# Kernel optimization log

Measured on AMD Instinct MI355X. Metric: run time of the kernel, lower is better.

The kernel has to match this reference:

```python
import jax, jax.numpy as jnp
import numpy as np

T, B, K = 512, 512, 8
V, H, NL, NLAB = 5, 30, 4, 3


def setup_inputs() -> dict:
    key = jax.random.key(0)
    ks = jax.random.split(key, 12)
    s = 0.1
    return {
        "x": jax.random.randint(ks[0], (T, B, K), 0, V),
        "weight_of_x": jax.random.uniform(ks[1], (T, B, K), dtype=jnp.float32),
        "embed": jax.random.normal(ks[2], (V, H), dtype=jnp.float32) * s,
        "lstm_Wih": jax.random.normal(ks[3], (NL, 4 * H, H), dtype=jnp.float32) * s,
        "lstm_Whh": jax.random.normal(ks[4], (NL, 4 * H, H), dtype=jnp.float32) * s,
        "lstm_bih": jax.random.normal(ks[5], (NL, 4 * H), dtype=jnp.float32) * s,
        "lstm_bhh": jax.random.normal(ks[6], (NL, 4 * H), dtype=jnp.float32) * s,
        "attn_W1": jax.random.normal(ks[7], (H, 64), dtype=jnp.float32) * s,
        "attn_b1": jnp.zeros((64,), jnp.float32),
        "attn_W2": jax.random.normal(ks[8], (64, 1), dtype=jnp.float32) * s,
        "attn_b2": jnp.zeros((1,), jnp.float32),
        "fc_W": jax.random.normal(ks[9], (H, NLAB), dtype=jnp.float32) * s,
        "fc_b": jnp.zeros((NLAB,), jnp.float32),
    }


def _lstm_layer(xs, Wih, Whh, bih, bhh):
    # xs: (T, B, H_in); PyTorch gate order i, f, g, o
    b = bih + bhh
    Bsz = xs.shape[1]
    h0 = jnp.zeros((Bsz, Whh.shape[1]), xs.dtype)

    def step(carry, xt):
        h, c = carry
        gates = xt @ Wih.T + h @ Whh.T + b  # (B, 4H)
        i, f, g, o = jnp.split(gates, 4, axis=-1)
        i, f, o = jax.nn.sigmoid(i), jax.nn.sigmoid(f), jax.nn.sigmoid(o)
        g = jnp.tanh(g)
        c = f * c + i * g
        h = o * jnp.tanh(c)
        return (h, c), h

    _, hs = jax.lax.scan(step, (h0, h0), xs)
    return hs  # (T, B, H)


def reference(x, weight_of_x, embed, lstm_Wih, lstm_Whh, lstm_bih, lstm_bhh,
              attn_W1, attn_b1, attn_W2, attn_b2, fc_W, fc_b):
    # embedding + weighted mean pooling over K
    e = embed[x] * weight_of_x[..., None]          # (T, B, K, H)
    e = jax.nn.relu(e)
    seq = jnp.mean(e, axis=2)                      # (T, B, H)

    # 4-layer LSTM (loop over fixed num_layers)
    out = seq
    for l in range(lstm_Wih.shape[0]):
        out = _lstm_layer(out, lstm_Wih[l], lstm_Whh[l], lstm_bih[l], lstm_bhh[l])

    # attention pooling over time
    enc = jnp.transpose(out, (1, 0, 2))            # (B, T, H)
    energy = jax.nn.relu(enc @ attn_W1 + attn_b1) @ attn_W2 + attn_b2  # (B, T, 1)
    weights = jax.nn.softmax(energy[..., 0], axis=1)  # (B, T)
    pooled = jnp.sum(enc * weights[..., None], axis=1)  # (B, H)

    # dropout is identity in eval mode
    logit = jax.nn.softmax(pooled @ fc_W + fc_b, axis=1)  # (B, 3)
    return logit
```

## Files before the change

### kernel.cpp

```cpp
#include <hip/hip_runtime.h>

#define TT 512
#define BB 512
#define KK 8
#define HH 30
#define GG 120
#define NLAYER 4

typedef _Float16 half2v __attribute__((ext_vector_type(2)));

__device__ __forceinline__ float rcp_f(float x) { return __builtin_amdgcn_rcpf(x); }
__device__ __forceinline__ float rdlane_f(float v, int l) {
    return __int_as_float(__builtin_amdgcn_readlane(__float_as_int(v), l));
}
__device__ __forceinline__ unsigned int rdlane_u(unsigned int v, int l) {
    return (unsigned int)__builtin_amdgcn_readlane((int)v, l);
}
__device__ __forceinline__ half2v as_h2(unsigned int u) {
    union { unsigned int u; half2v h; } c; c.u = u; return c.h;
}
__device__ __forceinline__ float2 pk_fma_s(float2 a, float2 bs, float2 c) {
    float2 d;
    asm("v_pk_fma_f32 %0, %1, %2, %3" : "=v"(d) : "v"(a), "s"(bs), "v"(c));
    return d;
}
__device__ __forceinline__ float swap32_hi(float x) {
    float a = x, b = x;
    asm("v_permlane32_swap_b32 %0, %1" : "+v"(a), "+v"(b));
    return b;
}

__global__ __launch_bounds__(256) __attribute__((amdgpu_waves_per_eu(2, 2)))
void rnn_fused(
    const int*   __restrict__ xin,  const float* __restrict__ wxin,
    const float* __restrict__ embed,
    const float* __restrict__ Wih,  const float* __restrict__ Whh,
    const float* __restrict__ bih,  const float* __restrict__ bhh,
    const float* __restrict__ W1,   const float* __restrict__ b1,
    const float* __restrict__ W2,   const float* __restrict__ b2,
    const float* __restrict__ fcW,  const float* __restrict__ fcb,
    float* __restrict__ out)
{
    __shared__ alignas(16) float hstore[TT * HH];
    __shared__ alignas(16) unsigned int seqring16[2][16][16];
    __shared__ alignas(16) int   ringx[4][16][KK];
    __shared__ alignas(16) float ringw[4][16][KK];
    __shared__ alignas(16) unsigned int hring16[3][16][16];
    __shared__ alignas(16) float re_s[5 * HH];
    __shared__ alignas(16) float energy_s[TT];
    __shared__ float red_s[16];
    __shared__ float part_s[8][HH];
    __shared__ float pooled_s[HH];
    __shared__ float logits_s[3];
    __shared__ int   sync_s[8];

    const int tid  = threadIdx.x;
    const int wv   = tid >> 6;
    const int lane = tid & 63;
    const int b    = blockIdx.x;
    volatile int* vs = sync_s;

    if (tid < 8) sync_s[tid] = 0;
    if (tid < 5 * HH) re_s[tid] = fmaxf(embed[tid], 0.0f);

    int4 hx = {0,0,0,0}; float4 hw = {0,0,0,0};
    if (wv == 0 && lane < 32) {
        const int r = lane >> 1, hf = lane & 1;
        #pragma unroll
        for (int cc = 0; cc < 2; ++cc) {
            long off = ((long)(16 * cc + r) * BB + b) * KK + hf * 4;
            *(int4*)(&ringx[cc][r][hf * 4])   = *(const int4*)(xin  + off);
            *(float4*)(&ringw[cc][r][hf * 4]) = *(const float4*)(wxin + off);
        }
        long off2 = ((long)(32 + r) * BB + b) * KK + hf * 4;
        hx = *(const int4*)(xin  + off2);
        hw = *(const float4*)(wxin + off2);
    }

    const int half = lane >> 5;
    const int q31  = lane & 31;
    const int qq   = (q31 < HH) ? q31 : (HH - 1);
    const int rA   = qq + half * HH;
    const int rB   = rA + 60;
    half2v wihA_h[15], wihB_h[15], whhA_h[15], whhB_h[15];
    {
        const float* WihL = Wih + wv * GG * HH;
        const float* WhhL = Whh + wv * GG * HH;
        #pragma unroll
        for (int kk = 0; kk < 15; ++kk) {
            float2 a0 = *(const float2*)(WihL + rA * HH + 2 * kk);
            float2 a1 = *(const float2*)(WihL + rB * HH + 2 * kk);
            float2 a2 = *(const float2*)(WhhL + rA * HH + 2 * kk);
            float2 a3 = *(const float2*)(WhhL + rB * HH + 2 * kk);
            wihA_h[kk][0] = (_Float16)a0.x; wihA_h[kk][1] = (_Float16)a0.y;
            wihB_h[kk][0] = (_Float16)a1.x; wihB_h[kk][1] = (_Float16)a1.y;
            whhA_h[kk][0] = (_Float16)a2.x; whhA_h[kk][1] = (_Float16)a2.y;
            whhB_h[kk][0] = (_Float16)a3.x; whhB_h[kk][1] = (_Float16)a3.y;
        }
    }
    const float biasA = bih[wv * GG + rA] + bhh[wv * GG + rA];
    const float biasB = bih[wv * GG + rB] + bhh[wv * GG + rB];
    const float mBneg = (lane < 32) ? -2.0f : -1.0f;
    const float aB    = (lane < 32) ?  2.0f :  1.0f;
    const float dB    = (lane < 32) ? -1.0f :  0.0f;

    __syncthreads();

    float c_val = 0.0f;
    unsigned int hpk = 0;

    auto do_step = [&](int t) {
        const unsigned int* xsrc = (wv == 0) ? &seqring16[(t >> 4) & 1][t & 15][0]
                                             : &hring16[wv - 1][t & 15][0];
        uint4 q0 = ((const uint4*)xsrc)[0];
        uint4 q1 = ((const uint4*)xsrc)[1];
        uint4 q2 = ((const uint4*)xsrc)[2];
        uint4 q3 = ((const uint4*)xsrc)[3];
        const unsigned int xu[16] = {q0.x,q0.y,q0.z,q0.w, q1.x,q1.y,q1.z,q1.w,
                                     q2.x,q2.y,q2.z,q2.w, q3.x,q3.y,q3.z,q3.w};
        float ahA = 0.f, ahB = 0.f, ahA2 = 0.f, ahB2 = 0.f;
        #pragma unroll
        for (int k = 0; k < 8; ++k) {
            const half2v hp = as_h2(rdlane_u(hpk, 2 * k));
            ahA = __builtin_amdgcn_fdot2(whhA_h[k], hp, ahA, false);
            ahB = __builtin_amdgcn_fdot2(whhB_h[k], hp, ahB, false);
        }
        #pragma unroll
        for (int k = 8; k < 15; ++k) {
            const half2v hp = as_h2(rdlane_u(hpk, 2 * k));
            ahA2 = __builtin_amdgcn_fdot2(whhA_h[k], hp, ahA2, false);
            ahB2 = __builtin_amdgcn_fdot2(whhB_h[k], hp, ahB2, false);
        }
        float axA = 0.f, axB = 0.f;
        #pragma unroll
        for (int k = 0; k < 15; ++k) {
            const half2v xp = as_h2(xu[k]);
            axA = __builtin_amdgcn_fdot2(wihA_h[k], xp, axA, false);
            axB = __builtin_amdgcn_fdot2(wihB_h[k], xp, axB, false);
        }
        const float gA = (axA + ahA) + (ahA2 + biasA);
        const float gB = (axB + ahB) + (ahB2 + biasB);
        const float actA = rcp_f(1.0f + __expf(-gA));
        const float sB   = rcp_f(1.0f + __expf(gB * mBneg));
        const float actB = fmaf(aB, sB, dB);
        const float fI = swap32_hi(actA);
        const float oI = swap32_hi(actB);
        c_val = fmaf(fI, c_val, actA * actB);
        const float tC = fmaf(2.0f, rcp_f(1.0f + __expf(-2.0f * c_val)), -1.0f);
        const float hv = oI * tC;
        union { _Float16 f[2]; unsigned int u; } cv; cv.u = 0;
        cv.f[0] = (_Float16)hv;
        const unsigned int hu  = cv.u;
        const unsigned int hup = (unsigned int)__builtin_amdgcn_mov_dpp(
                                     (int)hu, 0xB1, 0xF, 0xF, true);
        hpk = hu | (hup << 16);
        if (lane < HH) {
            if (wv == NLAYER - 1) hstore[t * HH + lane] = hv;
            else if (!(lane & 1)) hring16[wv][t & 15][lane >> 1] = hpk;
        }
    };

    for (int T0 = 0; T0 < TT; T0 += 8) {
        if (wv == 0) {
            if ((T0 & 15) == 0) {
                const int c = T0 >> 4;
                if (lane < 32) {
                    const int r = lane >> 1, hf = lane & 1;
                    if (c <= 29) {
                        const int sl = (c + 2) & 3;
                        *(int4*)(&ringx[sl][r][hf * 4])   = hx;
                        *(float4*)(&ringw[sl][r][hf * 4]) = hw;
                    }
                    if (c <= 28) {
                        long off = ((long)(16 * (c + 3) + r) * BB + b) * KK + hf * 4;
                        hx = *(const int4*)(xin  + off);
                        hw = *(const float4*)(wxin + off);
                    }
                }
                const int sl = c & 3, par = c & 1;
                #pragma unroll
                for (int rr = 0; rr < 8; ++rr) {
                    const int o = lane + rr * 64;
                    if (o < 480) {
                        const int tr = o / HH, j = o - tr * HH;
                        int4   xa = *(const int4*)(&ringx[sl][tr][0]);
                        int4   xb = *(const int4*)(&ringx[sl][tr][4]);
                        float4 wa = *(const float4*)(&ringw[sl][tr][0]);
                        float4 wb = *(const float4*)(&ringw[sl][tr][4]);
                        float acc = re_s[xa.x * HH + j] * wa.x;
                        acc = fmaf(re_s[xa.y * HH + j], wa.y, acc);
                        acc = fmaf(re_s[xa.z * HH + j], wa.z, acc);
                        acc = fmaf(re_s[xa.w * HH + j], wa.w, acc);
                        acc = fmaf(re_s[xb.x * HH + j], wb.x, acc);
                        acc = fmaf(re_s[xb.y * HH + j], wb.y, acc);
                        acc = fmaf(re_s[xb.z * HH + j], wb.z, acc);
                        acc = fmaf(re_s[xb.w * HH + j], wb.w, acc);
                        ((_Float16*)&seqring16[par][tr][0])[j] = (_Float16)(acc * 0.125f);
                    }
                }
                __threadfence_block();
            }
        } else {
            while (vs[wv - 1] < T0 + 8) __builtin_amdgcn_s_sleep(1);
        }
        if (wv < NLAYER - 1) {
            while (vs[4 + wv + 1] < T0 - 8) __builtin_amdgcn_s_sleep(1);
        }
        __threadfence_block();
        #pragma unroll 1
        for (int tt = 0; tt < 8; ++tt)
            do_step(T0 + tt);
        __threadfence_block();
        if (lane == 0) {
            if (wv < NLAYER - 1) vs[wv]     = T0 + 8;
            if (wv > 0)          vs[4 + wv] = T0 + 8;
        }
    }

    __syncthreads();

    {
        const float* W1p = W1;
        const float* b1p = b1;
        const float* W2p = W2;
        asm volatile("" : "+v"(W1p), "+v"(b1p), "+v"(W2p));

        float w1cx[15], w1cy[15];
        #pragma unroll
        for (int k = 0; k < 15; ++k) {
            w1cx[k] = W1p[(2 * k) * 64 + lane];
            w1cy[k] = W1p[(2 * k + 1) * 64 + lane];
        }
        const float b1v = b1p[lane];
        const float w2v = W2p[lane];
        const float b2v = b2[0];
        #pragma unroll
        for (int pass = 0; pass < 2; ++pass) {
            const int t = wv * 128 + pass * 64 + lane;
            float2 h2[15];
            #pragma unroll
            for (int k = 0; k < 15; ++k)
                h2[k] = *(const float2*)(hstore + t * HH + 2 * k);
            float e = b2v;
            for (int u = 0; u < 64; ++u) {
                float2 acc = {0.f, 0.f};
                #pragma unroll
                for (int k = 0; k < 15; ++k) {
                    float2 wp;
                    wp.x = rdlane_f(w1cx[k], u);
                    wp.y = rdlane_f(w1cy[k], u);
                    acc = pk_fma_s(h2[k], wp, acc);
                }
                const float su = acc.x + acc.y + rdlane_f(b1v, u);
                e = fmaf(fmaxf(su, 0.0f), rdlane_f(w2v, u), e);
            }
            energy_s[t] = e;
        }
    }
    __syncthreads();

    float mx = -3.0e38f;
    for (int i = tid; i < TT; i += 256) mx = fmaxf(mx, energy_s[i]);
    #pragma unroll
    for (int m = 1; m < 64; m <<= 1) mx = fmaxf(mx, __shfl_xor(mx, m, 64));
    if (lane == 0) red_s[wv] = mx;
    __syncthreads();
    mx = fmaxf(fmaxf(red_s[0], red_s[1]), fmaxf(red_s[2], red_s[3]));
    float ssum = 0.0f;
    for (int i = tid; i < TT; i += 256) {
        float ev = __expf(energy_s[i] - mx);
        energy_s[i] = ev;
        ssum += ev;
    }
    #pragma unroll
    for (int m = 1; m < 64; m <<= 1) ssum += __shfl_xor(ssum, m, 64);
    if (lane == 0) red_s[8 + wv] = ssum;
    __syncthreads();
    const float invS = rcp_f(red_s[8] + red_s[9] + red_s[10] + red_s[11]);

    {
        const int g = tid >> 5, jj = tid & 31;
        if (jj < HH) {
            float part = 0.0f;
            for (int t = g; t < TT; t += 8)
                part = fmaf(energy_s[t] * invS, hstore[t * HH + jj], part);
            part_s[g][jj] = part;
        }
    }
    __syncthreads();
    if (tid < HH) {
        float pv = 0.0f;
        #pragma unroll
        for (int q = 0; q < 8; ++q) pv += part_s[q][tid];
        pooled_s[tid] = pv;
    }
    __syncthreads();

    if (tid < 3) {
        float acc = fcb[tid];
        #pragma unroll
        for (int k = 0; k < HH; ++k) acc = fmaf(pooled_s[k], fcW[k * 3 + tid], acc);
        logits_s[tid] = acc;
    }
    __syncthreads();
    if (tid == 0) {
        float l0 = logits_s[0], l1 = logits_s[1], l2 = logits_s[2];
        float m3 = fmaxf(l0, fmaxf(l1, l2));
        float e0 = __expf(l0 - m3), e1 = __expf(l1 - m3), e2 = __expf(l2 - m3);
        float inv = rcp_f(e0 + e1 + e2);
        out[b * 3 + 0] = e0 * inv; out[b * 3 + 1] = e1 * inv; out[b * 3 + 2] = e2 * inv;
    }
}

extern "C" void kernel_launch(void* const* d_in, const int* in_sizes, int n_in,
                              void* d_out, int out_size, void* d_ws, size_t ws_size,
                              hipStream_t stream)
{
    (void)in_sizes; (void)n_in; (void)d_ws; (void)ws_size; (void)out_size;
    rnn_fused<<<BB, 256, 0, stream>>>(
        (const int*)  d_in[0],  (const float*)d_in[1],  (const float*)d_in[2],
        (const float*)d_in[3],  (const float*)d_in[4],  (const float*)d_in[5],
        (const float*)d_in[6],  (const float*)d_in[7],  (const float*)d_in[8],
        (const float*)d_in[9],  (const float*)d_in[10], (const float*)d_in[11],
        (const float*)d_in[12], (float*)d_out);
}
```

Measured before the change: 442.5 us.

## Split into embed, MFMA-batched wavefront-pipelined LSTM, and attention kernels

Replaces the single per-sequence fused kernel with three kernels. An embedding kernel writes pooled inputs as fp16 to workspace. An LSTM kernel handles 16 sequences per block, computing gates with fp16 MFMA 16x16x32 and folding the bias into an augmented input column. Its four waves each own one layer and run as a layer-wavefront pipeline through LDS rings. The change aims to replace scalar per-sequence recurrence math with matrix-core batching, at the cost of workspace traffic, only 32 blocks in the recurrent kernel, and fp16 precision in gate inputs; the old kernel remains as a fallback when no workspace is given.

```diff
diff --git a/kernel.cpp b/kernel.cpp
--- a/kernel.cpp
+++ b/kernel.cpp
@@ -7,23 +7,315 @@
 #define GG 120
 #define NLAYER 4
 
-typedef _Float16 half2v __attribute__((ext_vector_type(2)));
+#define SPB16 16
+#define NB1   (BB / SPB16)
+
+typedef _Float16 f16x8 __attribute__((ext_vector_type(8)));
+typedef float    f32x4 __attribute__((ext_vector_type(4)));
 
 __device__ __forceinline__ float rcp_f(float x) { return __builtin_amdgcn_rcpf(x); }
 __device__ __forceinline__ float rdlane_f(float v, int l) {
     return __int_as_float(__builtin_amdgcn_readlane(__float_as_int(v), l));
-}
-__device__ __forceinline__ unsigned int rdlane_u(unsigned int v, int l) {
-    return (unsigned int)__builtin_amdgcn_readlane((int)v, l);
-}
-__device__ __forceinline__ half2v as_h2(unsigned int u) {
-    union { unsigned int u; half2v h; } c; c.u = u; return c.h;
 }
 __device__ __forceinline__ float2 pk_fma_s(float2 a, float2 bs, float2 c) {
     float2 d;
     asm("v_pk_fma_f32 %0, %1, %2, %3" : "=v"(d) : "v"(a), "s"(bs), "v"(c));
     return d;
 }
+__device__ __forceinline__ float sigf(float x) {
+    return rcp_f(1.0f + __expf(-x));
+}
+__device__ __forceinline__ float tanhf_fast(float x) {
+    return fmaf(2.0f, rcp_f(1.0f + __expf(-2.0f * x)), -1.0f);
+}
+__device__ __forceinline__ unsigned int cvt_pk_u(float a, float b) {
+    auto h = __builtin_amdgcn_cvt_pkrtz(a, b);
+    union { decltype(h) h2; unsigned int u; } c; c.h2 = h; return c.u;
+}
+
+__global__ __launch_bounds__(256) void k0_embed(
+    const int* __restrict__ xin, const float* __restrict__ wxin,
+    const float* __restrict__ embed, unsigned int* __restrict__ wsx)
+{
+    const unsigned int idx = blockIdx.x * 256 + threadIdx.x;
+    const int p   = idx & 15;
+    const int s   = (idx >> 4) & 15;
+    const int t   = (idx >> 8) & 511;
+    const int blk = idx >> 17;
+    if (p == 15) { wsx[idx] = 0x00003C00u; return; }
+    const int b = blk * SPB16 + s;
+    const long base = ((long)t * BB + b) * KK;
+    int4   xa = *(const int4*)(xin + base);
+    int4   xb = *(const int4*)(xin + base + 4);
+    float4 wa = *(const float4*)(wxin + base);
+    float4 wb = *(const float4*)(wxin + base + 4);
+    const int hid0 = 2 * p;
+    float a0 = 0.f, a1 = 0.f;
+    const int   xv[8] = {xa.x, xa.y, xa.z, xa.w, xb.x, xb.y, xb.z, xb.w};
+    const float wv[8] = {wa.x, wa.y, wa.z, wa.w, wb.x, wb.y, wb.z, wb.w};
+    #pragma unroll
+    for (int k = 0; k < 8; ++k) {
+        float2 e2 = *(const float2*)(embed + xv[k] * HH + hid0);
+        a0 = fmaf(wv[k], fmaxf(e2.x, 0.f), a0);
+        a1 = fmaf(wv[k], fmaxf(e2.y, 0.f), a1);
+    }
+    wsx[idx] = cvt_pk_u(a0 * 0.125f, a1 * 0.125f);
+}
+
+__global__ __launch_bounds__(256) __attribute__((amdgpu_waves_per_eu(1, 1)))
+void k1_lstm(
+    const unsigned int* __restrict__ wsx,
+    const float* __restrict__ Wih, const float* __restrict__ Whh,
+    const float* __restrict__ bih, const float* __restrict__ bhh,
+    float* __restrict__ wsh)
+{
+    __shared__ alignas(16) uint4 ring[NLAYER - 1][16][64];
+
+    const int tid  = threadIdx.x;
+    const int wv   = tid >> 6;
+    const int lane = tid & 63;
+    const int q    = lane >> 4;
+    const int s    = lane & 15;
+    const int blk  = blockIdx.x;
+
+    f16x8 wihF[8], whhF[8];
+    {
+        const float* WihL = Wih + wv * GG * HH;
+        const float* WhhL = Whh + wv * GG * HH;
+        const int m = lane & 15;
+        #pragma unroll
+        for (int t8 = 0; t8 < 8; ++t8) {
+            const int h_idx = 8 * (m >> 2) + 4 * (t8 & 1) + (m & 3);
+            const int gate  = t8 >> 1;
+            const bool vrow = (h_idx < HH);
+            const int r_eff = gate * HH + (vrow ? h_idx : 0);
+            const float bsum = bih[wv * GG + r_eff] + bhh[wv * GG + r_eff];
+            #pragma unroll
+            for (int e = 0; e < 8; ++e) {
+                const int k = q * 8 + e;
+                float wh = (vrow && k < HH) ? WhhL[r_eff * HH + k] : 0.0f;
+                float wi = 0.0f;
+                if (vrow) {
+                    if (k < HH)       wi = WihL[r_eff * HH + k];
+                    else if (k == HH) wi = bsum;
+                }
+                whhF[t8][e] = (_Float16)wh;
+                wihF[t8][e] = (_Float16)wi;
+            }
+        }
+    }
+
+    __syncthreads();
+
+    uint4 hBu;
+    hBu.x = 0u; hBu.y = 0u; hBu.z = 0u; hBu.w = (q == 3) ? 0x00003C00u : 0u;
+    float c[8];
+    #pragma unroll
+    for (int e = 0; e < 8; ++e) c[e] = 0.0f;
+
+    const f32x4 zed = {0.f, 0.f, 0.f, 0.f};
+    const int NGROUP = TT / 8;
+    const int NEPOCH = NGROUP + NLAYER - 1;
+
+    for (int n = 0; n < NEPOCH; ++n) {
+        const int g = n - wv;
+        if (g >= 0 && g < NGROUP) {
+            const int T0 = 8 * g;
+            uint4 xq[8];
+            if (wv == 0) {
+                const uint4* xp = (const uint4*)wsx;
+                #pragma unroll
+                for (int j = 0; j < 8; ++j)
+                    xq[j] = xp[((long)(blk * TT + T0 + j) * SPB16 + s) * 4 + q];
+            } else {
+                #pragma unroll
+                for (int j = 0; j < 8; ++j)
+                    xq[j] = ring[wv - 1][(T0 + j) & 15][lane];
+            }
+            #pragma unroll
+            for (int j = 0; j < 8; ++j) {
+                const int t = T0 + j;
+                union { uint4 u; f16x8 h; } xc; xc.u = xq[j];
+                union { uint4 u; f16x8 h; } hc; hc.u = hBu;
+                f32x4 acc[8];
+                #pragma unroll
+                for (int i = 0; i < 8; ++i)
+                    acc[i] = __builtin_amdgcn_mfma_f32_16x16x32_f16(
+                                 wihF[i], xc.h, zed, 0, 0, 0);
+                #pragma unroll
+                for (int i = 0; i < 8; ++i)
+                    acc[i] = __builtin_amdgcn_mfma_f32_16x16x32_f16(
+                                 whhF[i], hc.h, acc[i], 0, 0, 0);
+                float h[8];
+                #pragma unroll
+                for (int e = 0; e < 8; ++e) {
+                    const int t2 = e >> 2, r = e & 3;
+                    const float gi = acc[0 + t2][r];
+                    const float gf = acc[2 + t2][r];
+                    const float gg = acc[4 + t2][r];
+                    const float go = acc[6 + t2][r];
+                    const float iv = sigf(gi);
+                    const float fv = sigf(gf);
+                    const float gv = tanhf_fast(gg);
+                    const float ov = sigf(go);
+                    c[e] = fmaf(fv, c[e], iv * gv);
+                    h[e] = ov * tanhf_fast(c[e]);
+                }
+                hBu.x = cvt_pk_u(h[0], h[1]);
+                hBu.y = cvt_pk_u(h[2], h[3]);
+                hBu.z = cvt_pk_u(h[4], h[5]);
+                hBu.w = (q == 3) ? 0x00003C00u : cvt_pk_u(h[6], h[7]);
+                if (wv < NLAYER - 1) {
+                    ring[wv][t & 15][lane] = hBu;
+                } else {
+                    float* dst = wsh + (((long)(blk * TT + t) * SPB16 + s) * 32 + 8 * q);
+                    float4 s0 = {h[0], h[1], h[2], h[3]};
+                    float4 s1 = {h[4], h[5], h[6], h[7]};
+                    *(float4*)dst       = s0;
+                    *(float4*)(dst + 4) = s1;
+                }
+            }
+        }
+        __syncthreads();
+    }
+}
+
+__global__ __launch_bounds__(256) void k2_attn(
+    const float* __restrict__ wsh,
+    const float* __restrict__ W1, const float* __restrict__ b1,
+    const float* __restrict__ W2, const float* __restrict__ b2,
+    const float* __restrict__ fcW, const float* __restrict__ fcb,
+    float* __restrict__ out)
+{
+    __shared__ alignas(16) float hst[TT * HH];
+    __shared__ alignas(16) float energy_s[TT];
+    __shared__ float red_s[16];
+    __shared__ float part_s[8][HH];
+    __shared__ float pooled_s[HH];
+    __shared__ float logits_s[3];
+
+    const int tid  = threadIdx.x;
+    const int wv   = tid >> 6;
+    const int lane = tid & 63;
+    const int b    = blockIdx.x;
+    const int blk  = b >> 4;
+    const int s    = b & 15;
+
+    #pragma unroll
+    for (int i = 0; i < 16; ++i) {
+        const int u  = tid + 256 * i;
+        const int t  = u >> 3;
+        const int sl = u & 7;
+        float4 v = *(const float4*)(wsh +
+                     (((long)(blk * TT + t) * SPB16 + s) * 32 + sl * 4));
+        const int hid = sl * 4;
+        if (sl < 7) {
+            hst[t * HH + hid + 0] = v.x;
+            hst[t * HH + hid + 1] = v.y;
+            hst[t * HH + hid + 2] = v.z;
+            hst[t * HH + hid + 3] = v.w;
+        } else {
+            hst[t * HH + 28] = v.x;
+            hst[t * HH + 29] = v.y;
+        }
+    }
+    __syncthreads();
+
+    {
+        float w1cx[15], w1cy[15];
+        #pragma unroll
+        for (int k = 0; k < 15; ++k) {
+            w1cx[k] = W1[(2 * k) * 64 + lane];
+            w1cy[k] = W1[(2 * k + 1) * 64 + lane];
+        }
+        const float b1v = b1[lane];
+        const float w2v = W2[lane];
+        const float b2v = b2[0];
+        #pragma unroll
+        for (int pass = 0; pass < 2; ++pass) {
+            const int t = wv * 128 + pass * 64 + lane;
+            float2 h2[15];
+            #pragma unroll
+            for (int k = 0; k < 15; ++k)
+                h2[k] = *(const float2*)(hst + t * HH + 2 * k);
+            float e = b2v;
+            for (int u = 0; u < 64; ++u) {
+                float2 acc = {0.f, 0.f};
+                #pragma unroll
+                for (int k = 0; k < 15; ++k) {
+                    float2 wp;
+                    wp.x = rdlane_f(w1cx[k], u);
+                    wp.y = rdlane_f(w1cy[k], u);
+                    acc = pk_fma_s(h2[k], wp, acc);
+                }
+                const float su = acc.x + acc.y + rdlane_f(b1v, u);
+                e = fmaf(fmaxf(su, 0.0f), rdlane_f(w2v, u), e);
+            }
+            energy_s[t] = e;
+        }
+    }
+    __syncthreads();
+
+    float mx = -3.0e38f;
+    for (int i = tid; i < TT; i += 256) mx = fmaxf(mx, energy_s[i]);
+    #pragma unroll
+    for (int m = 1; m < 64; m <<= 1) mx = fmaxf(mx, __shfl_xor(mx, m, 64));
+    if (lane == 0) red_s[wv] = mx;
+    __syncthreads();
+    mx = fmaxf(fmaxf(red_s[0], red_s[1]), fmaxf(red_s[2], red_s[3]));
+    float ssum = 0.0f;
+    for (int i = tid; i < TT; i += 256) {
+        float ev = __expf(energy_s[i] - mx);
+        energy_s[i] = ev;
+        ssum += ev;
+    }
+    #pragma unroll
+    for (int m = 1; m < 64; m <<= 1) ssum += __shfl_xor(ssum, m, 64);
+    if (lane == 0) red_s[8 + wv] = ssum;
+    __syncthreads();
+    const float invS = rcp_f(red_s[8] + red_s[9] + red_s[10] + red_s[11]);
+
+    {
+        const int g = tid >> 5, jj = tid & 31;
+        if (jj < HH) {
+            float part = 0.0f;
+            for (int t = g; t < TT; t += 8)
+                part = fmaf(energy_s[t] * invS, hst[t * HH + jj], part);
+            part_s[g][jj] = part;
+        }
+    }
+    __syncthreads();
+    if (tid < HH) {
+        float pv = 0.0f;
+        #pragma unroll
+        for (int qq = 0; qq < 8; ++qq) pv += part_s[qq][tid];
+        pooled_s[tid] = pv;
+    }
+    __syncthreads();
+
+    if (tid < 3) {
+        float acc = fcb[tid];
+        #pragma unroll
+        for (int k = 0; k < HH; ++k) acc = fmaf(pooled_s[k], fcW[k * 3 + tid], acc);
+        logits_s[tid] = acc;
+    }
+    __syncthreads();
+    if (tid == 0) {
+        float l0 = logits_s[0], l1 = logits_s[1], l2 = logits_s[2];
+        float m3 = fmaxf(l0, fmaxf(l1, l2));
+        float e0 = __expf(l0 - m3), e1 = __expf(l1 - m3), e2 = __expf(l2 - m3);
+        float inv = rcp_f(e0 + e1 + e2);
+        out[b * 3 + 0] = e0 * inv; out[b * 3 + 1] = e1 * inv; out[b * 3 + 2] = e2 * inv;
+    }
+}
+
+typedef _Float16 half2v __attribute__((ext_vector_type(2)));
+__device__ __forceinline__ unsigned int rdlane_u(unsigned int v, int l) {
+    return (unsigned int)__builtin_amdgcn_readlane((int)v, l);
+}
+__device__ __forceinline__ half2v as_h2(unsigned int u) {
+    union { unsigned int u; half2v h; } c; c.u = u; return c.h;
+}
 __device__ __forceinline__ float swap32_hi(float x) {
     float a = x, b = x;
     asm("v_permlane32_swap_b32 %0, %1" : "+v"(a), "+v"(b));
@@ -31,7 +323,7 @@
 }
 
 __global__ __launch_bounds__(256) __attribute__((amdgpu_waves_per_eu(2, 2)))
-void rnn_fused(
+void rnn_fused_r8(
     const int*   __restrict__ xin,  const float* __restrict__ wxin,
     const float* __restrict__ embed,
     const float* __restrict__ Wih,  const float* __restrict__ Whh,
@@ -291,7 +583,7 @@
     if (tid < HH) {
         float pv = 0.0f;
         #pragma unroll
-        for (int q = 0; q < 8; ++q) pv += part_s[q][tid];
+        for (int q2 = 0; q2 < 8; ++q2) pv += part_s[q2][tid];
         pooled_s[tid] = pv;
     }
     __syncthreads();
@@ -316,11 +608,27 @@
                               void* d_out, int out_size, void* d_ws, size_t ws_size,
                               hipStream_t stream)
 {
-    (void)in_sizes; (void)n_in; (void)d_ws; (void)ws_size; (void)out_size;
-    rnn_fused<<<BB, 256, 0, stream>>>(
-        (const int*)  d_in[0],  (const float*)d_in[1],  (const float*)d_in[2],
-        (const float*)d_in[3],  (const float*)d_in[4],  (const float*)d_in[5],
-        (const float*)d_in[6],  (const float*)d_in[7],  (const float*)d_in[8],
-        (const float*)d_in[9],  (const float*)d_in[10], (const float*)d_in[11],
-        (const float*)d_in[12], (float*)d_out);
-}
+    (void)in_sizes; (void)n_in; (void)out_size;
+    const size_t WS_X = (size_t)NB1 * TT * SPB16 * 16 * 4;
+    const size_t WS_H = (size_t)NB1 * TT * SPB16 * 32 * 4;
+    if (d_ws != nullptr && ws_size >= WS_X + WS_H) {
+        unsigned int* wsx = (unsigned int*)d_ws;
+        float*        wsh = (float*)((char*)d_ws + WS_X);
+        k0_embed<<<(NB1 * TT * SPB16 * 16) / 256, 256, 0, stream>>>(
+            (const int*)d_in[0], (const float*)d_in[1], (const float*)d_in[2], wsx);
+        k1_lstm<<<NB1, 256, 0, stream>>>(
+            wsx, (const float*)d_in[3], (const float*)d_in[4],
+            (const float*)d_in[5], (const float*)d_in[6], wsh);
+        k2_attn<<<BB, 256, 0, stream>>>(
+            wsh, (const float*)d_in[7], (const float*)d_in[8],
+            (const float*)d_in[9], (const float*)d_in[10],
+            (const float*)d_in[11], (const float*)d_in[12], (float*)d_out);
+    } else {
+        rnn_fused_r8<<<BB, 256, 0, stream>>>(
+            (const int*)  d_in[0],  (const float*)d_in[1],  (const float*)d_in[2],
+            (const float*)d_in[3],  (const float*)d_in[4],  (const float*)d_in[5],
+            (const float*)d_in[6],  (const float*)d_in[7],  (const float*)d_in[8],
+            (const float*)d_in[9],  (const float*)d_in[10], (const float*)d_in[11],
+            (const float*)d_in[12], (float*)d_out);
+    }
+}
```

Measured after the change: 569.1 us. +28.6%, slower.
